# Performance work log

Measured on AMD Instinct MI355X. Metric: run time of the kernel, lower is better.

The kernel has to match this reference:

```python
import jax, jax.numpy as jnp
import numpy as np

N_NODES = 100000

def _gcn_norm(edge_index, num_nodes):
    # add self loops, compute symmetric normalization D^-1/2 (A+I) D^-1/2
    loops = jnp.arange(num_nodes, dtype=edge_index.dtype)
    row = jnp.concatenate([edge_index[0], loops])
    col = jnp.concatenate([edge_index[1], loops])
    ones = jnp.ones(row.shape[0], dtype=jnp.float32)
    deg = jax.ops.segment_sum(ones, row, num_segments=num_nodes)
    dinv = jnp.where(deg > 0, jax.lax.rsqrt(deg), 0.0)
    norm = dinv[row] * dinv[col]  # [E+N]
    return row, col, norm

def _gcn_conv(x, W, b, row, col, norm, num_nodes):
    h = x @ W                      # [N, out]
    msg = h[col] * norm[:, None]   # gather + scale, [E+N, out]
    out = jax.ops.segment_sum(msg, row, num_segments=num_nodes)
    return out + b

def setup_inputs() -> dict:
    key = jax.random.key(0)
    k1, k2, k3, k4 = jax.random.split(key, 4)
    F_IN, HID, CLS = 128, 128, 40
    E = 1_600_000
    x = jax.random.normal(k1, (N_NODES, F_IN), dtype=jnp.float32)
    edge_index = jax.random.randint(k2, (2, E), 0, N_NODES, dtype=jnp.int64)
    W1 = jax.random.normal(k3, (F_IN, HID), dtype=jnp.float32) / np.sqrt(F_IN)
    b1 = jnp.zeros((HID,), dtype=jnp.float32)
    W2 = jax.random.normal(k4, (HID, CLS), dtype=jnp.float32) / np.sqrt(HID)
    b2 = jnp.zeros((CLS,), dtype=jnp.float32)
    return {"x": x, "edge_index": edge_index, "W1": W1, "b1": b1, "W2": W2, "b2": b2}

def reference(x, edge_index, W1, b1, W2, b2):
    num_nodes = x.shape[0]
    row, col, norm = _gcn_norm(edge_index, num_nodes)
    h = _gcn_conv(x, W1, b1, row, col, norm, num_nodes)
    h = jax.nn.relu(h)
    h = _gcn_conv(h, W2, b2, row, col, norm, num_nodes)
    return jax.nn.log_softmax(h, axis=1)
```

## Files before the change

kernel.cpp:

```cpp
#include <hip/hip_runtime.h>
#include <hip/hip_bf16.h>
#include <math.h>


#define TILE_A 8192
#define RB 98
#define CAP 2048

typedef __attribute__((ext_vector_type(8))) short bf16x8;
typedef __attribute__((ext_vector_type(4))) float f32x4;
typedef __attribute__((ext_vector_type(2))) float f32x2;
typedef __attribute__((ext_vector_type(4))) unsigned int u32x4;

struct f8 { float v[8]; };

__device__ inline f8 unpack8(uint4 u) {
    f8 r;
    r.v[0] = __uint_as_float(u.x << 16);
    r.v[1] = __uint_as_float(u.x & 0xffff0000u);
    r.v[2] = __uint_as_float(u.y << 16);
    r.v[3] = __uint_as_float(u.y & 0xffff0000u);
    r.v[4] = __uint_as_float(u.z << 16);
    r.v[5] = __uint_as_float(u.z & 0xffff0000u);
    r.v[6] = __uint_as_float(u.w << 16);
    r.v[7] = __uint_as_float(u.w & 0xffff0000u);
    return r;
}

__device__ inline f8 unpack8f8(unsigned long long v) {
    f8 r;
#if __has_builtin(__builtin_amdgcn_cvt_pk_f32_fp8)
    int lo = (int)(unsigned)(v & 0xffffffffULL);
    int hi = (int)(unsigned)(v >> 32);
    f32x2 p0 = __builtin_amdgcn_cvt_pk_f32_fp8(lo, false);
    f32x2 p1 = __builtin_amdgcn_cvt_pk_f32_fp8(lo, true);
    f32x2 p2 = __builtin_amdgcn_cvt_pk_f32_fp8(hi, false);
    f32x2 p3 = __builtin_amdgcn_cvt_pk_f32_fp8(hi, true);
    r.v[0] = p0[0]; r.v[1] = p0[1]; r.v[2] = p1[0]; r.v[3] = p1[1];
    r.v[4] = p2[0]; r.v[5] = p2[1]; r.v[6] = p3[0]; r.v[7] = p3[1];
#else
#pragma unroll
    for (int k = 0; k < 8; ++k) {
        unsigned b = (unsigned)((v >> (8 * k)) & 0xffULL);
        unsigned em = b & 0x7f;
        unsigned bits = (em ? ((em << 20) + 0x3C000000u) : 0u) | ((b >> 7) << 31);
        r.v[k] = __uint_as_float(bits);
    }
#endif
    return r;
}

__device__ inline unsigned char fp8_of(float f) {
#if __has_builtin(__builtin_amdgcn_cvt_pk_fp8_f32)
    int p = __builtin_amdgcn_cvt_pk_fp8_f32(f, f, 0, false);
    return (unsigned char)(p & 0xff);
#else
    unsigned s = __float_as_uint(f) >> 31;
    float af = fabsf(f);
    if (af < 0.015625f) return (unsigned char)(s << 7);
    if (af > 448.f) af = 448.f;
    unsigned u = __float_as_uint(af);
    unsigned mant = (u >> 20) & 0x7;
    unsigned rest = u & 0xfffff;
    unsigned em = (((u >> 23) - 120) << 3) | mant;
    if (rest > 0x80000 || (rest == 0x80000 && (mant & 1))) em += 1;
    if (em > 0x7e) em = 0x7e;
    return (unsigned char)((s << 7) | em);
#endif
}

__device__ inline unsigned pack2(float a, float b) {
    __hip_bfloat16 ha = __float2bfloat16(a);
    __hip_bfloat16 hb = __float2bfloat16(b);
    unsigned short sa = *(unsigned short*)&ha;
    unsigned short sb = *(unsigned short*)&hb;
    return (unsigned)sa | ((unsigned)sb << 16);
}

__device__ inline short bfs(float f) {
    __hip_bfloat16 h = __float2bfloat16(f);
    return *(short*)&h;
}

__device__ inline bf16x8 to8(float4 p, float4 q) {
    bf16x8 v;
    v[0] = bfs(p.x); v[1] = bfs(p.y); v[2] = bfs(p.z); v[3] = bfs(p.w);
    v[4] = bfs(q.x); v[5] = bfs(q.y); v[6] = bfs(q.z); v[7] = bfs(q.w);
    return v;
}

__device__ inline int ecol_of(long long v) { return (int)(unsigned)(v & 0xffffffffLL); }
__device__ inline float ew_of(long long v) { return __int_as_float((int)(v >> 32)); }

__global__ __launch_bounds__(256) void k_wt(const float* __restrict__ W1,
                                            const float* __restrict__ W2,
                                            short* __restrict__ Wt1,
                                            short* __restrict__ Wt2,
                                            int* __restrict__ bktcnt) {
    int idx = blockIdx.x * 256 + threadIdx.x;
    if (idx < 16384) {
        int k = idx >> 7, f = idx & 127;
        Wt1[f * 128 + k] = bfs(W1[k * 128 + f]);
    } else if (idx < 16384 + 6144) {
        int j = idx - 16384;
        int f = j >> 7, k = j & 127;
        Wt2[j] = (f < 40) ? bfs(W2[k * 40 + f]) : (short)0;
    } else if (idx < 16384 + 6144 + 1024) {
        bktcnt[idx - 16384 - 6144] = 0;
    }
}

__global__ __launch_bounds__(1024) void k_binA(const int* __restrict__ ei,
                                               int* __restrict__ bktcnt,
                                               int2* __restrict__ brec, int E) {
    __shared__ int h[1024];
    __shared__ int cur[1024];
    int t = threadIdx.x;
    h[t] = 0;
    __syncthreads();
    int base = blockIdx.x * TILE_A;
    int lim = min(base + TILE_A, E);
    for (int i = base + t; i < lim; i += 1024) atomicAdd(&h[ei[i] / RB], 1);
    __syncthreads();
    cur[t] = h[t] ? atomicAdd(&bktcnt[t], h[t]) : 0;
    __syncthreads();
    for (int i = base + t; i < lim; i += 1024) {
        int r = ei[i];
        int b = r / RB;
        int pos = atomicAdd(&cur[b], 1);
        if (pos < CAP) brec[(size_t)b * CAP + pos] = make_int2(r, ei[E + i]);
    }
}

__global__ __launch_bounds__(256) void k_count3(const int2* __restrict__ brec,
                                                const int* __restrict__ bktcnt,
                                                int* __restrict__ deg, int N) {
    __shared__ int h[RB];
    int k = blockIdx.x;
    int t = threadIdx.x;
    if (t < RB) h[t] = 0;
    __syncthreads();
    int s = k * CAP;
    int e = s + min(bktcnt[k], CAP);
    int r0 = k * RB;
    for (int i = s + t; i < e; i += 256) atomicAdd(&h[brec[i].x - r0], 1);
    __syncthreads();
    if (t < RB && r0 + t < N) deg[r0 + t] = h[t] + 1;
}

__global__ __launch_bounds__(256) void k_scan1(const int* __restrict__ deg,
                                               int* __restrict__ tmp,
                                               int* __restrict__ bsum,
                                               float* __restrict__ dinv, int N) {
    __shared__ int l[256];
    int t = threadIdx.x;
    int i = blockIdx.x * 256 + t;
    int d = (i < N) ? deg[i] : 1;
    if (i < N) dinv[i] = rsqrtf((float)d);
    l[t] = (i < N) ? d - 1 : 0;
    __syncthreads();
#pragma unroll
    for (int o = 1; o < 256; o <<= 1) {
        int u = (t >= o) ? l[t - o] : 0;
        __syncthreads();
        l[t] += u;
        __syncthreads();
    }
    if (i < N) tmp[i] = l[t];
    if (t == 255) bsum[blockIdx.x] = l[255];
}

__global__ __launch_bounds__(1024) void k_scan2(int* __restrict__ bsum, int nb) {
    __shared__ int l[1024];
    int t = threadIdx.x;
    l[t] = (t < nb) ? bsum[t] : 0;
    __syncthreads();
#pragma unroll
    for (int o = 1; o < 1024; o <<= 1) {
        int u = (t >= o) ? l[t - o] : 0;
        __syncthreads();
        l[t] += u;
        __syncthreads();
    }
    if (t < nb) bsum[t] = l[t];
}

__global__ __launch_bounds__(256) void k_scan3(const int* __restrict__ deg,
                                               const int* __restrict__ tmp,
                                               const int* __restrict__ bsum,
                                               int* __restrict__ row_ptr, int N, int E) {
    int i = blockIdx.x * 256 + threadIdx.x;
    if (i >= N) return;
    int excl = tmp[i] - (deg[i] - 1) + (blockIdx.x ? bsum[blockIdx.x - 1] : 0);
    row_ptr[i] = excl;
    if (i == 0) row_ptr[N] = E;
}

__global__ __launch_bounds__(256) void k_csr3(const int2* __restrict__ brec,
                                              const int* __restrict__ bktcnt,
                                              const int* __restrict__ row_ptr,
                                              const float* __restrict__ dinv,
                                              long long* __restrict__ erec, int N) {
    __shared__ int cur[RB];
    int k = blockIdx.x;
    int t = threadIdx.x;
    int r0 = k * RB;
    if (t < RB) cur[t] = (r0 + t < N) ? row_ptr[r0 + t] : 0;
    __syncthreads();
    int s = k * CAP;
    int e = s + min(bktcnt[k], CAP);
    for (int i = s + t; i < e; i += 256) {
        int2 rc = brec[i];
        int pos = atomicAdd(&cur[rc.x - r0], 1);
        float w = dinv[rc.x] * dinv[rc.y];
        long long rec = (long long)((unsigned long long)(unsigned)__float_as_int(w) << 32) |
                        (unsigned long long)(unsigned)rc.y;
        erec[pos] = rec;
    }
}

__global__ __launch_bounds__(256) void k_gemm1m(const float* __restrict__ x,
                                                const short* __restrict__ Wt,
                                                unsigned char* __restrict__ Tf8, int N) {
    int t = threadIdx.x;
    int wid = t >> 6, l = t & 63;
    int r = l & 15;
    int ko = (l >> 4) * 8;
    long long nb = (long long)blockIdx.x * 128 + wid * 32;

    bf16x8 a[2][4];
#pragma unroll
    for (int g = 0; g < 2; ++g) {
        long long n = nb + g * 16 + r;
        if (n >= N) n = N - 1;
        const float* xr = x + n * 128;
#pragma unroll
        for (int kc = 0; kc < 4; ++kc) {
            float4 p = *(const float4*)(xr + kc * 32 + ko);
            float4 q = *(const float4*)(xr + kc * 32 + ko + 4);
            a[g][kc] = to8(p, q);
        }
    }

    f32x4 acc[2][8];
#pragma unroll
    for (int g = 0; g < 2; ++g)
#pragma unroll
        for (int ft = 0; ft < 8; ++ft) acc[g][ft] = (f32x4){0.f, 0.f, 0.f, 0.f};

#pragma unroll
    for (int ft = 0; ft < 8; ++ft) {
        const short* wp = Wt + (ft * 16 + r) * 128 + ko;
#pragma unroll
        for (int kc = 0; kc < 4; ++kc) {
            bf16x8 b = *(const bf16x8*)(wp + kc * 32);
            acc[0][ft] = __builtin_amdgcn_mfma_f32_16x16x32_bf16(a[0][kc], b, acc[0][ft], 0, 0, 0);
            acc[1][ft] = __builtin_amdgcn_mfma_f32_16x16x32_bf16(a[1][kc], b, acc[1][ft], 0, 0, 0);
        }
    }

    int row0 = (l >> 4) * 4;
#pragma unroll
    for (int g = 0; g < 2; ++g) {
#pragma unroll
        for (int i = 0; i < 4; ++i) {
            long long n = nb + g * 16 + row0 + i;
            if (n < N) {
                unsigned char* orow = Tf8 + n * 128;
#pragma unroll
                for (int ft = 0; ft < 8; ++ft) orow[ft * 16 + r] = fp8_of(acc[g][ft][i]);
            }
        }
    }
}

__global__ __launch_bounds__(256) void k_gemm2m(const short* __restrict__ Ub,
                                                const short* __restrict__ Wt2,
                                                short* __restrict__ H2a,
                                                short* __restrict__ H2c, int N) {
    int t = threadIdx.x;
    int wid = t >> 6, l = t & 63;
    int r = l & 15;
    int ko = (l >> 4) * 8;
    long long nb = (long long)blockIdx.x * 128 + wid * 32;

    bf16x8 a[2][4];
#pragma unroll
    for (int g = 0; g < 2; ++g) {
        long long n = nb + g * 16 + r;
        if (n >= N) n = N - 1;
        const short* ur = Ub + n * 128;
#pragma unroll
        for (int kc = 0; kc < 4; ++kc)
            a[g][kc] = *(const bf16x8*)(ur + kc * 32 + ko);
    }

    f32x4 acc[2][3];
#pragma unroll
    for (int g = 0; g < 2; ++g)
#pragma unroll
        for (int ft = 0; ft < 3; ++ft) acc[g][ft] = (f32x4){0.f, 0.f, 0.f, 0.f};

#pragma unroll
    for (int ft = 0; ft < 3; ++ft) {
        const short* wp = Wt2 + (ft * 16 + r) * 128 + ko;
#pragma unroll
        for (int kc = 0; kc < 4; ++kc) {
            bf16x8 b = *(const bf16x8*)(wp + kc * 32);
            acc[0][ft] = __builtin_amdgcn_mfma_f32_16x16x32_bf16(a[0][kc], b, acc[0][ft], 0, 0, 0);
            acc[1][ft] = __builtin_amdgcn_mfma_f32_16x16x32_bf16(a[1][kc], b, acc[1][ft], 0, 0, 0);
        }
    }

    int row0 = (l >> 4) * 4;
#pragma unroll
    for (int g = 0; g < 2; ++g) {
#pragma unroll
        for (int i = 0; i < 4; ++i) {
            long long n = nb + g * 16 + row0 + i;
            if (n < N) {
#pragma unroll
                for (int ft = 0; ft < 3; ++ft) {
                    int f = ft * 16 + r;
                    if (f < 32) H2a[n * 32 + f] = bfs(acc[g][ft][i]);
                    else if (f < 40) H2c[n * 8 + (f - 32)] = bfs(acc[g][ft][i]);
                }
            }
        }
    }
}

__global__ __launch_bounds__(256) void k_pull1(const unsigned long long* __restrict__ T8,
                                               const float* __restrict__ dinv,
                                               const int* __restrict__ row_ptr,
                                               const long long* __restrict__ erec,
                                               const float* __restrict__ b,
                                               uint4* __restrict__ Ub, int N) {
    int tid = blockIdx.x * 256 + threadIdx.x;
    int n = tid >> 4;
    if (n >= N) return;
    int q = tid & 15;

    float dn = dinv[n];
    float ss = dn * dn;
    f8 s8 = unpack8f8(T8[(size_t)n * 16 + q]);
    float acc[8];
#pragma unroll
    for (int j = 0; j < 8; ++j) acc[j] = s8.v[j] * ss;

    int beg = row_ptr[n], end = row_ptr[n + 1];
    int i = beg;
    for (; i + 3 < end; i += 4) {
        long long e0 = __builtin_nontemporal_load(erec + i);
        long long e1 = __builtin_nontemporal_load(erec + i + 1);
        long long e2 = __builtin_nontemporal_load(erec + i + 2);
        long long e3 = __builtin_nontemporal_load(erec + i + 3);
        unsigned long long g0 = T8[(size_t)ecol_of(e0) * 16 + q];
        unsigned long long g1 = T8[(size_t)ecol_of(e1) * 16 + q];
        unsigned long long g2 = T8[(size_t)ecol_of(e2) * 16 + q];
        unsigned long long g3 = T8[(size_t)ecol_of(e3) * 16 + q];
        float w0 = ew_of(e0);
        float w1 = ew_of(e1);
        float w2 = ew_of(e2);
        float w3 = ew_of(e3);
        f8 a0 = unpack8f8(g0);
        f8 a1 = unpack8f8(g1);
        f8 a2 = unpack8f8(g2);
        f8 a3 = unpack8f8(g3);
#pragma unroll
        for (int j = 0; j < 8; ++j) acc[j] = fmaf(w0, a0.v[j], acc[j]);
#pragma unroll
        for (int j = 0; j < 8; ++j) acc[j] = fmaf(w1, a1.v[j], acc[j]);
#pragma unroll
        for (int j = 0; j < 8; ++j) acc[j] = fmaf(w2, a2.v[j], acc[j]);
#pragma unroll
        for (int j = 0; j < 8; ++j) acc[j] = fmaf(w3, a3.v[j], acc[j]);
    }
    for (; i < end; ++i) {
        long long e0 = __builtin_nontemporal_load(erec + i);
        float w0 = ew_of(e0);
        f8 a0 = unpack8f8(T8[(size_t)ecol_of(e0) * 16 + q]);
#pragma unroll
        for (int j = 0; j < 8; ++j) acc[j] = fmaf(w0, a0.v[j], acc[j]);
    }

    float4 b0 = ((const float4*)b)[q * 2];
    float4 b1v = ((const float4*)b)[q * 2 + 1];
    acc[0] = fmaxf(acc[0] + b0.x, 0.f);
    acc[1] = fmaxf(acc[1] + b0.y, 0.f);
    acc[2] = fmaxf(acc[2] + b0.z, 0.f);
    acc[3] = fmaxf(acc[3] + b0.w, 0.f);
    acc[4] = fmaxf(acc[4] + b1v.x, 0.f);
    acc[5] = fmaxf(acc[5] + b1v.y, 0.f);
    acc[6] = fmaxf(acc[6] + b1v.z, 0.f);
    acc[7] = fmaxf(acc[7] + b1v.w, 0.f);

    uint4 o;
    o.x = pack2(acc[0], acc[1]);
    o.y = pack2(acc[2], acc[3]);
    o.z = pack2(acc[4], acc[5]);
    o.w = pack2(acc[6], acc[7]);
    Ub[(size_t)n * 16 + q] = o;
}

__global__ __launch_bounds__(256) void k_pull2(const uint4* __restrict__ H2a4,
                                               const uint4* __restrict__ H2c4,
                                               const float* __restrict__ dinv,
                                               const int* __restrict__ row_ptr,
                                               const long long* __restrict__ erec,
                                               const float* __restrict__ b2,
                                               float* __restrict__ out, int N) {
    int tid = blockIdx.x * 256 + threadIdx.x;
    int n = tid >> 3;
    if (n >= N) return;
    int q = tid & 7;
    bool act = q < 5;
    bool ina = q < 4;
    const uint4* bp = ina ? (H2a4 + q) : H2c4;
    size_t stride = ina ? 4 : 1;

    float dn = dinv[n];
    float ss = dn * dn;
    float acc[8];
#pragma unroll
    for (int j = 0; j < 8; ++j) acc[j] = 0.f;
    if (act) {
        f8 s8 = unpack8(bp[(size_t)n * stride]);
#pragma unroll
        for (int j = 0; j < 8; ++j) acc[j] = s8.v[j] * ss;
    }
    int beg = row_ptr[n], end = row_ptr[n + 1];
    int i = beg;
    for (; i + 3 < end; i += 4) {
        long long e0 = __builtin_nontemporal_load(erec + i);
        long long e1 = __builtin_nontemporal_load(erec + i + 1);
        long long e2 = __builtin_nontemporal_load(erec + i + 2);
        long long e3 = __builtin_nontemporal_load(erec + i + 3);
        uint4 g0 = bp[(size_t)ecol_of(e0) * stride];
        uint4 g1 = bp[(size_t)ecol_of(e1) * stride];
        uint4 g2 = bp[(size_t)ecol_of(e2) * stride];
        uint4 g3 = bp[(size_t)ecol_of(e3) * stride];
        if (act) {
            float w0 = ew_of(e0), w1 = ew_of(e1), w2 = ew_of(e2), w3 = ew_of(e3);
            f8 a0 = unpack8(g0);
            f8 a1 = unpack8(g1);
            f8 a2 = unpack8(g2);
            f8 a3 = unpack8(g3);
#pragma unroll
            for (int j = 0; j < 8; ++j) acc[j] = fmaf(w0, a0.v[j], acc[j]);
#pragma unroll
            for (int j = 0; j < 8; ++j) acc[j] = fmaf(w1, a1.v[j], acc[j]);
#pragma unroll
            for (int j = 0; j < 8; ++j) acc[j] = fmaf(w2, a2.v[j], acc[j]);
#pragma unroll
            for (int j = 0; j < 8; ++j) acc[j] = fmaf(w3, a3.v[j], acc[j]);
        }
    }
    for (; i < end; ++i) {
        long long e0 = erec[i];
        if (act) {
            float w0 = ew_of(e0);
            f8 a0 = unpack8(bp[(size_t)ecol_of(e0) * stride]);
#pragma unroll
            for (int j = 0; j < 8; ++j) acc[j] = fmaf(w0, a0.v[j], acc[j]);
        }
    }
    if (act) {
        float4 b0 = ((const float4*)b2)[q * 2];
        float4 b1v = ((const float4*)b2)[q * 2 + 1];
        acc[0] += b0.x; acc[1] += b0.y; acc[2] += b0.z; acc[3] += b0.w;
        acc[4] += b1v.x; acc[5] += b1v.y; acc[6] += b1v.z; acc[7] += b1v.w;
    }
    float m = -INFINITY;
    if (act) {
#pragma unroll
        for (int j = 0; j < 8; ++j) m = fmaxf(m, acc[j]);
    }
#pragma unroll
    for (int o = 4; o > 0; o >>= 1) m = fmaxf(m, __shfl_xor(m, o, 8));
    float e = 0.f;
    if (act) {
#pragma unroll
        for (int j = 0; j < 8; ++j) e += expf(acc[j] - m);
    }
#pragma unroll
    for (int o = 4; o > 0; o >>= 1) e += __shfl_xor(e, o, 8);
    float lg = m + logf(e);
    if (act) {
        float4* o4 = (float4*)out;
        o4[(size_t)n * 10 + q * 2] =
            make_float4(acc[0] - lg, acc[1] - lg, acc[2] - lg, acc[3] - lg);
        o4[(size_t)n * 10 + q * 2 + 1] =
            make_float4(acc[4] - lg, acc[5] - lg, acc[6] - lg, acc[7] - lg);
    }
}

extern "C" void kernel_launch(void* const* d_in, const int* in_sizes, int n_in,
                              void* d_out, int out_size, void* d_ws, size_t ws_size,
                              hipStream_t stream) {
    const float* x  = (const float*)d_in[0];
    const int*   ei = (const int*)d_in[1];
    const float* W1 = (const float*)d_in[2];
    const float* b1 = (const float*)d_in[3];
    const float* W2 = (const float*)d_in[4];
    const float* b2 = (const float*)d_in[5];
    float* out = (float*)d_out;

    const int N = in_sizes[0] / 128;
    const int E = in_sizes[1] / 2;
    const int nbkt = (N + RB - 1) / RB;

    char* ws = (char*)d_ws;
    int*   deg     = (int*)(ws);
    float* dinv    = (float*)(ws + (512 << 10));
    int*   row_ptr = (int*)(ws + (1 << 20));
    int*   bsum    = (int*)(ws + (1536 << 10));
    int*   tmp     = (int*)(ws + (1600 << 10));
    int*   bktcnt  = (int*)(ws + (2100 << 10));
    short* Wt1     = (short*)(ws + (2200 << 10));
    short* Wt2     = (short*)(ws + (2300 << 10));
    long long* erec = (long long*)(ws + (3 << 20));
    int2*  brec    = (int2*)(ws + (16 << 20));
    short* H2a     = (short*)(ws + (33 << 20));
    short* H2c     = (short*)(ws + (40 << 20));
    unsigned char* Tf8 = (unsigned char*)(ws + (42 << 20));
    unsigned* Ub   = (unsigned*)(ws + (55 << 20));

    int nb = (N + 255) / 256;
    int na = (E + TILE_A - 1) / TILE_A;
    int ng = (N + 127) / 128;

    k_wt<<<92, 256, 0, stream>>>(W1, W2, Wt1, Wt2, bktcnt);
    k_binA<<<na, 1024, 0, stream>>>(ei, bktcnt, brec, E);
    k_count3<<<nbkt, 256, 0, stream>>>(brec, bktcnt, deg, N);
    k_scan1<<<nb, 256, 0, stream>>>(deg, tmp, bsum, dinv, N);
    k_scan2<<<1, 1024, 0, stream>>>(bsum, nb);
    k_scan3<<<nb, 256, 0, stream>>>(deg, tmp, bsum, row_ptr, N, E);
    k_csr3<<<nbkt, 256, 0, stream>>>(brec, bktcnt, row_ptr, dinv, erec, N);

    k_gemm1m<<<ng, 256, 0, stream>>>(x, Wt1, Tf8, N);
    k_pull1<<<((long long)N * 16 + 255) / 256, 256, 0, stream>>>(
        (const unsigned long long*)Tf8, dinv, row_ptr, erec, b1, (uint4*)Ub, N);
    k_gemm2m<<<ng, 256, 0, stream>>>((const short*)Ub, Wt2, H2a, H2c, N);
    k_pull2<<<((long long)N * 8 + 255) / 256, 256, 0, stream>>>(
        (const uint4*)H2a, (const uint4*)H2c, dinv, row_ptr, erec, b2, out, N);
}
```

Before: 187.3 us.

## Replace global CSR prefix scan with per-bucket local offsets and widen pull1 unroll

The three-kernel global prefix scan (scan1/scan2/scan3) is removed. Each bucket's count kernel now does a local scan and writes per-row (begin,end) pairs into a bucket-padded edge array, with CAP slots per bucket. It also computes dinv in the same kernel. This removes three launches and their global passes, at the cost of a sparser erec layout with gaps between buckets. The pull1 gather loop also gains an 8-way unrolled main loop to keep more gathers in flight.

Measured after the change: 177.7 us, median of 2. 1.05x faster.

```diff
diff --git a/kernel.cpp b/kernel.cpp
--- a/kernel.cpp
+++ b/kernel.cpp
@@ -132,10 +132,12 @@
     }
 }
 
-__global__ __launch_bounds__(256) void k_count3(const int2* __restrict__ brec,
-                                                const int* __restrict__ bktcnt,
-                                                int* __restrict__ deg, int N) {
+__global__ __launch_bounds__(256) void k_cnt(const int2* __restrict__ brec,
+                                             const int* __restrict__ bktcnt,
+                                             int2* __restrict__ rbe,
+                                             float* __restrict__ dinv, int N) {
     __shared__ int h[RB];
+    __shared__ int l[256];
     int k = blockIdx.x;
     int t = threadIdx.x;
     if (t < RB) h[t] = 0;
@@ -145,19 +147,8 @@
     int r0 = k * RB;
     for (int i = s + t; i < e; i += 256) atomicAdd(&h[brec[i].x - r0], 1);
     __syncthreads();
-    if (t < RB && r0 + t < N) deg[r0 + t] = h[t] + 1;
-}
-
-__global__ __launch_bounds__(256) void k_scan1(const int* __restrict__ deg,
-                                               int* __restrict__ tmp,
-                                               int* __restrict__ bsum,
-                                               float* __restrict__ dinv, int N) {
-    __shared__ int l[256];
-    int t = threadIdx.x;
-    int i = blockIdx.x * 256 + t;
-    int d = (i < N) ? deg[i] : 1;
-    if (i < N) dinv[i] = rsqrtf((float)d);
-    l[t] = (i < N) ? d - 1 : 0;
+    int v = (t < RB) ? h[t] : 0;
+    l[t] = v;
     __syncthreads();
 #pragma unroll
     for (int o = 1; o < 256; o <<= 1) {
@@ -166,46 +157,23 @@
         l[t] += u;
         __syncthreads();
     }
-    if (i < N) tmp[i] = l[t];
-    if (t == 255) bsum[blockIdx.x] = l[255];
-}
-
-__global__ __launch_bounds__(1024) void k_scan2(int* __restrict__ bsum, int nb) {
-    __shared__ int l[1024];
-    int t = threadIdx.x;
-    l[t] = (t < nb) ? bsum[t] : 0;
-    __syncthreads();
-#pragma unroll
-    for (int o = 1; o < 1024; o <<= 1) {
-        int u = (t >= o) ? l[t - o] : 0;
-        __syncthreads();
-        l[t] += u;
-        __syncthreads();
-    }
-    if (t < nb) bsum[t] = l[t];
-}
-
-__global__ __launch_bounds__(256) void k_scan3(const int* __restrict__ deg,
-                                               const int* __restrict__ tmp,
-                                               const int* __restrict__ bsum,
-                                               int* __restrict__ row_ptr, int N, int E) {
-    int i = blockIdx.x * 256 + threadIdx.x;
-    if (i >= N) return;
-    int excl = tmp[i] - (deg[i] - 1) + (blockIdx.x ? bsum[blockIdx.x - 1] : 0);
-    row_ptr[i] = excl;
-    if (i == 0) row_ptr[N] = E;
+    if (t < RB && r0 + t < N) {
+        int beg = s + (l[t] - v);
+        rbe[r0 + t] = make_int2(beg, beg + v);
+        dinv[r0 + t] = rsqrtf((float)(v + 1));
+    }
 }
 
 __global__ __launch_bounds__(256) void k_csr3(const int2* __restrict__ brec,
                                               const int* __restrict__ bktcnt,
-                                              const int* __restrict__ row_ptr,
+                                              const int2* __restrict__ rbe,
                                               const float* __restrict__ dinv,
                                               long long* __restrict__ erec, int N) {
     __shared__ int cur[RB];
     int k = blockIdx.x;
     int t = threadIdx.x;
     int r0 = k * RB;
-    if (t < RB) cur[t] = (r0 + t < N) ? row_ptr[r0 + t] : 0;
+    if (t < RB) cur[t] = (r0 + t < N) ? rbe[r0 + t].x : 0;
     __syncthreads();
     int s = k * CAP;
     int e = s + min(bktcnt[k], CAP);
@@ -332,7 +300,7 @@
 
 __global__ __launch_bounds__(256) void k_pull1(const unsigned long long* __restrict__ T8,
                                                const float* __restrict__ dinv,
-                                               const int* __restrict__ row_ptr,
+                                               const int2* __restrict__ rbe,
                                                const long long* __restrict__ erec,
                                                const float* __restrict__ b,
                                                uint4* __restrict__ Ub, int N) {
@@ -348,8 +316,52 @@
 #pragma unroll
     for (int j = 0; j < 8; ++j) acc[j] = s8.v[j] * ss;
 
-    int beg = row_ptr[n], end = row_ptr[n + 1];
-    int i = beg;
+    int2 be = rbe[n];
+    int i = be.x, end = be.y;
+    for (; i + 7 < end; i += 8) {
+        long long e0 = __builtin_nontemporal_load(erec + i);
+        long long e1 = __builtin_nontemporal_load(erec + i + 1);
+        long long e2 = __builtin_nontemporal_load(erec + i + 2);
+        long long e3 = __builtin_nontemporal_load(erec + i + 3);
+        long long e4 = __builtin_nontemporal_load(erec + i + 4);
+        long long e5 = __builtin_nontemporal_load(erec + i + 5);
+        long long e6 = __builtin_nontemporal_load(erec + i + 6);
+        long long e7 = __builtin_nontemporal_load(erec + i + 7);
+        unsigned long long g0 = T8[(size_t)ecol_of(e0) * 16 + q];
+        unsigned long long g1 = T8[(size_t)ecol_of(e1) * 16 + q];
+        unsigned long long g2 = T8[(size_t)ecol_of(e2) * 16 + q];
+        unsigned long long g3 = T8[(size_t)ecol_of(e3) * 16 + q];
+        unsigned long long g4 = T8[(size_t)ecol_of(e4) * 16 + q];
+        unsigned long long g5 = T8[(size_t)ecol_of(e5) * 16 + q];
+        unsigned long long g6 = T8[(size_t)ecol_of(e6) * 16 + q];
+        unsigned long long g7 = T8[(size_t)ecol_of(e7) * 16 + q];
+        f8 a0 = unpack8f8(g0);
+        f8 a1 = unpack8f8(g1);
+        f8 a2 = unpack8f8(g2);
+        f8 a3 = unpack8f8(g3);
+        f8 a4 = unpack8f8(g4);
+        f8 a5 = unpack8f8(g5);
+        f8 a6 = unpack8f8(g6);
+        f8 a7 = unpack8f8(g7);
+        float w0 = ew_of(e0), w1 = ew_of(e1), w2 = ew_of(e2), w3 = ew_of(e3);
+        float w4 = ew_of(e4), w5 = ew_of(e5), w6 = ew_of(e6), w7 = ew_of(e7);
+#pragma unroll
+        for (int j = 0; j < 8; ++j) acc[j] = fmaf(w0, a0.v[j], acc[j]);
+#pragma unroll
+        for (int j = 0; j < 8; ++j) acc[j] = fmaf(w1, a1.v[j], acc[j]);
+#pragma unroll
+        for (int j = 0; j < 8; ++j) acc[j] = fmaf(w2, a2.v[j], acc[j]);
+#pragma unroll
+        for (int j = 0; j < 8; ++j) acc[j] = fmaf(w3, a3.v[j], acc[j]);
+#pragma unroll
+        for (int j = 0; j < 8; ++j) acc[j] = fmaf(w4, a4.v[j], acc[j]);
+#pragma unroll
+        for (int j = 0; j < 8; ++j) acc[j] = fmaf(w5, a5.v[j], acc[j]);
+#pragma unroll
+        for (int j = 0; j < 8; ++j) acc[j] = fmaf(w6, a6.v[j], acc[j]);
+#pragma unroll
+        for (int j = 0; j < 8; ++j) acc[j] = fmaf(w7, a7.v[j], acc[j]);
+    }
     for (; i + 3 < end; i += 4) {
         long long e0 = __builtin_nontemporal_load(erec + i);
         long long e1 = __builtin_nontemporal_load(erec + i + 1);
@@ -359,14 +371,11 @@
         unsigned long long g1 = T8[(size_t)ecol_of(e1) * 16 + q];
         unsigned long long g2 = T8[(size_t)ecol_of(e2) * 16 + q];
         unsigned long long g3 = T8[(size_t)ecol_of(e3) * 16 + q];
-        float w0 = ew_of(e0);
-        float w1 = ew_of(e1);
-        float w2 = ew_of(e2);
-        float w3 = ew_of(e3);
         f8 a0 = unpack8f8(g0);
         f8 a1 = unpack8f8(g1);
         f8 a2 = unpack8f8(g2);
         f8 a3 = unpack8f8(g3);
+        float w0 = ew_of(e0), w1 = ew_of(e1), w2 = ew_of(e2), w3 = ew_of(e3);
 #pragma unroll
         for (int j = 0; j < 8; ++j) acc[j] = fmaf(w0, a0.v[j], acc[j]);
 #pragma unroll
@@ -406,7 +415,7 @@
 __global__ __launch_bounds__(256) void k_pull2(const uint4* __restrict__ H2a4,
                                                const uint4* __restrict__ H2c4,
                                                const float* __restrict__ dinv,
-                                               const int* __restrict__ row_ptr,
+                                               const int2* __restrict__ rbe,
                                                const long long* __restrict__ erec,
                                                const float* __restrict__ b2,
                                                float* __restrict__ out, int N) {
@@ -429,8 +438,8 @@
 #pragma unroll
         for (int j = 0; j < 8; ++j) acc[j] = s8.v[j] * ss;
     }
-    int beg = row_ptr[n], end = row_ptr[n + 1];
-    int i = beg;
+    int2 be = rbe[n];
+    int i = be.x, end = be.y;
     for (; i + 3 < end; i += 4) {
         long long e0 = __builtin_nontemporal_load(erec + i);
         long long e1 = __builtin_nontemporal_load(erec + i + 1);
@@ -511,37 +520,30 @@
     const int nbkt = (N + RB - 1) / RB;
 
     char* ws = (char*)d_ws;
-    int*   deg     = (int*)(ws);
-    float* dinv    = (float*)(ws + (512 << 10));
-    int*   row_ptr = (int*)(ws + (1 << 20));
-    int*   bsum    = (int*)(ws + (1536 << 10));
-    int*   tmp     = (int*)(ws + (1600 << 10));
-    int*   bktcnt  = (int*)(ws + (2100 << 10));
-    short* Wt1     = (short*)(ws + (2200 << 10));
-    short* Wt2     = (short*)(ws + (2300 << 10));
+    float* dinv    = (float*)(ws);
+    int2*  rbe     = (int2*)(ws + (512 << 10));
+    int*   bktcnt  = (int*)(ws + (1536 << 10));
+    short* Wt1     = (short*)(ws + (1600 << 10));
+    short* Wt2     = (short*)(ws + (1700 << 10));
     long long* erec = (long long*)(ws + (3 << 20));
-    int2*  brec    = (int2*)(ws + (16 << 20));
-    short* H2a     = (short*)(ws + (33 << 20));
-    short* H2c     = (short*)(ws + (40 << 20));
-    unsigned char* Tf8 = (unsigned char*)(ws + (42 << 20));
-    unsigned* Ub   = (unsigned*)(ws + (55 << 20));
-
-    int nb = (N + 255) / 256;
+    int2*  brec    = (int2*)(ws + (21 << 20));
+    short* H2a     = (short*)(ws + (38 << 20));
+    short* H2c     = (short*)(ws + (45 << 20));
+    unsigned char* Tf8 = (unsigned char*)(ws + (47 << 20));
+    unsigned* Ub   = (unsigned*)(ws + (60 << 20));
+
     int na = (E + TILE_A - 1) / TILE_A;
     int ng = (N + 127) / 128;
 
     k_wt<<<92, 256, 0, stream>>>(W1, W2, Wt1, Wt2, bktcnt);
     k_binA<<<na, 1024, 0, stream>>>(ei, bktcnt, brec, E);
-    k_count3<<<nbkt, 256, 0, stream>>>(brec, bktcnt, deg, N);
-    k_scan1<<<nb, 256, 0, stream>>>(deg, tmp, bsum, dinv, N);
-    k_scan2<<<1, 1024, 0, stream>>>(bsum, nb);
-    k_scan3<<<nb, 256, 0, stream>>>(deg, tmp, bsum, row_ptr, N, E);
-    k_csr3<<<nbkt, 256, 0, stream>>>(brec, bktcnt, row_ptr, dinv, erec, N);
+    k_cnt<<<nbkt, 256, 0, stream>>>(brec, bktcnt, rbe, dinv, N);
+    k_csr3<<<nbkt, 256, 0, stream>>>(brec, bktcnt, rbe, dinv, erec, N);
 
     k_gemm1m<<<ng, 256, 0, stream>>>(x, Wt1, Tf8, N);
     k_pull1<<<((long long)N * 16 + 255) / 256, 256, 0, stream>>>(
-        (const unsigned long long*)Tf8, dinv, row_ptr, erec, b1, (uint4*)Ub, N);
+        (const unsigned long long*)Tf8, dinv, rbe, erec, b1, (uint4*)Ub, N);
     k_gemm2m<<<ng, 256, 0, stream>>>((const short*)Ub, Wt2, H2a, H2c, N);
     k_pull2<<<((long long)N * 8 + 255) / 256, 256, 0, stream>>>(
-        (const uint4*)H2a, (const uint4*)H2c, dinv, row_ptr, erec, b2, out, N);
-}
+        (const uint4*)H2a, (const uint4*)H2c, dinv, rbe, erec, b2, out, N);
+}
```
